# Kernel tuning notes

Hardware: AMD Instinct MI355X
Metric: run time of the kernel (lower is better)

## Reference

```python
import jax, jax.numpy as jnp
import numpy as np

EMBED_DIM = 1024
NUM_HEADS = 16
HEAD_DIM = EMBED_DIM // NUM_HEADS


def setup_inputs() -> dict:
    key = jax.random.key(0)
    ks = jax.random.split(key, 11)
    B, T, D = 4, 2048, EMBED_DIM
    s = 1.0 / np.sqrt(D)
    inp = {
        "x": jax.random.normal(ks[0], (B, T, D), dtype=jnp.float32),
        "wq": jax.random.normal(ks[1], (D, D), dtype=jnp.float32) * s,
        "bq": jnp.zeros((D,), dtype=jnp.float32),
        "wk": jax.random.normal(ks[2], (D, D), dtype=jnp.float32) * s,
        "bk": jnp.zeros((D,), dtype=jnp.float32),
        "wv": jax.random.normal(ks[3], (D, D), dtype=jnp.float32) * s,
        "bv": jnp.zeros((D,), dtype=jnp.float32),
        "wo": jax.random.normal(ks[4], (D, D), dtype=jnp.float32) * s,
        "bo": jnp.zeros((D,), dtype=jnp.float32),
        "ln_gamma": jnp.ones((D,), dtype=jnp.float32),
        "ln_beta": jnp.zeros((D,), dtype=jnp.float32),
    }
    return inp


def _attention(x, wq, bq, wk, bk, wv, bv, wo, bo, ln_gamma, ln_beta):
    B, T, D = x.shape
    H, Hd = NUM_HEADS, HEAD_DIM
    # projections -> (B, H, T, Hd)
    q = (x @ wq + bq).reshape(B, T, H, Hd).transpose(0, 2, 1, 3)
    k = (x @ wk + bk).reshape(B, T, H, Hd).transpose(0, 2, 1, 3)
    v = (x @ wv + bv).reshape(B, T, H, Hd).transpose(0, 2, 1, 3)
    scores = jnp.einsum("bhqd,bhkd->bhqk", q, k) / jnp.sqrt(jnp.asarray(Hd, x.dtype))
    attn = jax.nn.softmax(scores, axis=-1)  # dropout p=0 -> identity
    out = jnp.einsum("bhqk,bhkd->bhqd", attn, v)
    out = out.transpose(0, 2, 1, 3).reshape(B, T, D)
    out = out @ wo + bo
    # LayerNorm (no residual in the original forward)
    mu = jnp.mean(out, axis=-1, keepdims=True)
    var = jnp.var(out, axis=-1, keepdims=True)
    out = (out - mu) / jnp.sqrt(var + 1e-5) * ln_gamma + ln_beta
    return out


def reference(x, wq, bq, wk, bk, wv, bv, wo, bo, ln_gamma, ln_beta):
    return _attention(x, wq, bq, wk, bk, wv, bv, wo, bo, ln_gamma, ln_beta)
```

## Files before the change

kernel.cpp:

```cpp
#include <hip/hip_runtime.h>
#include <hip/hip_bf16.h>

typedef __bf16 bf16_t;
typedef __bf16 bf16x4v __attribute__((ext_vector_type(4)));
typedef __bf16 bf16x8 __attribute__((ext_vector_type(8)));
typedef float  f32x4  __attribute__((ext_vector_type(4)));

typedef __attribute__((address_space(1))) void* gptr_t;
typedef __attribute__((address_space(3))) void* lptr_t;

#define B_BATCH  4
#define T_SEQ    2048
#define D_MODEL  1024
#define N_HEADS  16
#define HEAD_DIM 64
#define M_ROWS   (B_BATCH * T_SEQ)

#define PROW 40

#define EXP2_SCALE 0.1803368801111204f

__global__ __launch_bounds__(256) void cvt_x(
    const float* __restrict__ in, bf16_t* __restrict__ out)
{
    const size_t tid = (size_t)blockIdx.x * 256 + threadIdx.x;
    for (int rep = 0; rep < 4; rep++) {
        const size_t i = (tid + (size_t)rep * 524288) * 4;
        const f32x4 v = *(const f32x4*)&in[i];
        bf16x4v o;
        for (int e = 0; e < 4; e++) o[e] = (bf16_t)v[e];
        *(bf16x4v*)&out[i] = o;
    }
}

__global__ __launch_bounds__(256) void transpose_w(
    const float* __restrict__ w0, const float* __restrict__ w1,
    const float* __restrict__ w2, const float* __restrict__ w3,
    bf16_t* __restrict__ out)
{
    __shared__ bf16_t tile[32][33];
    const int z = blockIdx.z;
    const float* w = (z == 0) ? w0 : (z == 1) ? w1 : (z == 2) ? w2 : w3;
    bf16_t* o = out + (size_t)z * D_MODEL * D_MODEL;
    const int tx = threadIdx.x & 31, ty = threadIdx.x >> 5;
    const int k0 = blockIdx.y * 32, n0 = blockIdx.x * 32;
    for (int i = 0; i < 4; i++)
        tile[ty + i * 8][tx] = (bf16_t)w[(size_t)(k0 + ty + i * 8) * D_MODEL + n0 + tx];
    __syncthreads();
    for (int i = 0; i < 4; i++)
        o[(size_t)(n0 + ty + i * 8) * D_MODEL + k0 + tx] = tile[tx][ty + i * 8];
}

__global__ __launch_bounds__(512, 2) void qkv_k(
    const bf16_t* __restrict__ A, const bf16_t* __restrict__ BT,
    const float* __restrict__ bq, const float* __restrict__ bk,
    const float* __restrict__ bv,
    bf16_t* __restrict__ qk_out, bf16_t* __restrict__ vt_out)
{
    __shared__ __attribute__((aligned(16))) bf16_t smem[49152];

    const int tid = threadIdx.x;
    const int f0 = blockIdx.y * 24 + blockIdx.x;
    const int f  = (f0 & 7) * 96 + (f0 >> 3);
    const int n_t = f % 24, m_t = f / 24;
    const int m0 = m_t * 256, n0 = n_t * 128;
    const int z  = n0 >> 10;
    const int w = tid >> 6, lane = tid & 63, quad = lane >> 4, l16 = lane & 15;
    const int wm = w >> 1, wn = w & 1;
    const int srow = lane >> 3;
    const int scol = ((lane & 7) ^ srow) * 8;
    const int rx = l16 & 7;

    f32x4 acc[4][4] = {};

    for (int it = 0; it < 4; it++) {
        const int R = w * 32 + it * 8;
        __builtin_amdgcn_global_load_lds(
            (gptr_t)&A[(size_t)(m0 + R + srow) * D_MODEL + scol],
            (lptr_t)&smem[R * 64], 16, 0, 0);
    }
    for (int it = 0; it < 2; it++) {
        const int R = w * 16 + it * 8;
        __builtin_amdgcn_global_load_lds(
            (gptr_t)&BT[(size_t)(n0 + R + srow) * D_MODEL + scol],
            (lptr_t)&smem[32768 + R * 64], 16, 0, 0);
    }

    for (int t = 0; t < 16; t++) {
        __syncthreads();
        const bf16_t* Ac = &smem[(t & 1) * 16384];
        const bf16_t* Bc = &smem[32768 + (t & 1) * 8192];
        bf16_t* An = &smem[((t + 1) & 1) * 16384];
        bf16_t* Bn = &smem[32768 + ((t + 1) & 1) * 8192];
        const int kb = (t + 1) * 64;
        const bool pf = (t + 1 < 16);

        #pragma unroll
        for (int s = 0; s < 2; s++) {
            const int rc = ((quad + s * 4) ^ rx) * 8;
            bf16x8 bfr[4];
            #pragma unroll
            for (int j = 0; j < 4; j++)
                bfr[j] = *(const bf16x8*)&Bc[(wn * 64 + j * 16 + l16) * 64 + rc];
            if (pf) {
                const int RA0 = w * 32 + (s * 2) * 8;
                __builtin_amdgcn_global_load_lds(
                    (gptr_t)&A[(size_t)(m0 + RA0 + srow) * D_MODEL + kb + scol],
                    (lptr_t)&An[RA0 * 64], 16, 0, 0);
                const int RA1 = w * 32 + (s * 2 + 1) * 8;
                __builtin_amdgcn_global_load_lds(
                    (gptr_t)&A[(size_t)(m0 + RA1 + srow) * D_MODEL + kb + scol],
                    (lptr_t)&An[RA1 * 64], 16, 0, 0);
                const int RB = w * 16 + s * 8;
                __builtin_amdgcn_global_load_lds(
                    (gptr_t)&BT[(size_t)(n0 + RB + srow) * D_MODEL + kb + scol],
                    (lptr_t)&Bn[RB * 64], 16, 0, 0);
            }
            bf16x8 af[4];
            #pragma unroll
            for (int i = 0; i < 4; i++)
                af[i] = *(const bf16x8*)&Ac[(wm * 64 + i * 16 + l16) * 64 + rc];
            __builtin_amdgcn_s_setprio(1);
            #pragma unroll
            for (int i = 0; i < 4; i++)
                #pragma unroll
                for (int j = 0; j < 4; j++)
                    acc[i][j] = __builtin_amdgcn_mfma_f32_16x16x32_bf16(
                        af[i], bfr[j], acc[i][j], 0, 0, 0);
            __builtin_amdgcn_s_setprio(0);
        }
    }

    __syncthreads();

    const float* bias = (z == 0) ? bq : (z == 1) ? bk : bv;
    const float qscale = (z == 0) ? EXP2_SCALE : 1.0f;
    const int ncol0 = n0 & 1023;
    float bj[4];
    for (int j = 0; j < 4; j++)
        bj[j] = bias[ncol0 + wn * 64 + j * 16 + l16];

    const int bidx = m0 >> 11, t0 = m0 & 2047, hbase = ncol0 >> 6;
    if (z < 2) {
        bf16_t (*Cs)[136] = reinterpret_cast<bf16_t(*)[136]>(smem);
        for (int ai = 0; ai < 4; ai++)
            for (int r = 0; r < 4; r++) {
                const int row = wm * 64 + ai * 16 + quad * 4 + r;
                for (int j = 0; j < 4; j++)
                    Cs[row][wn * 64 + j * 16 + l16] =
                        (bf16_t)((acc[ai][j][r] + bj[j]) * qscale);
            }
        __syncthreads();
        bf16_t* outp = qk_out + (size_t)z * ((size_t)M_ROWS * D_MODEL);
        for (int p = 0; p < 8; p++) {
            const int chunk = p * 512 + tid;
            const int sub = chunk & 15, tt = chunk >> 4;
            const int hl = sub >> 3, sub8 = sub & 7;
            const bf16x8 val = *(const bf16x8*)&Cs[tt][hl * 64 + sub8 * 8];
            *(bf16x8*)&outp[(((size_t)(bidx * N_HEADS + hbase + hl)) * T_SEQ + t0 + tt)
                            * HEAD_DIM + sub8 * 8] = val;
        }
    } else {
        bf16_t (*CsV)[264] = reinterpret_cast<bf16_t(*)[264]>(smem);
        for (int ai = 0; ai < 4; ai++)
            for (int r = 0; r < 4; r++) {
                const int row = wm * 64 + ai * 16 + quad * 4 + r;
                for (int j = 0; j < 4; j++)
                    CsV[wn * 64 + j * 16 + l16][row] = (bf16_t)(acc[ai][j][r] + bj[j]);
            }
        __syncthreads();
        for (int p = 0; p < 8; p++) {
            const int chunk = p * 512 + tid;
            const int sub = chunk & 31, r = chunk >> 5;
            const int h = hbase + (r >> 6), hd = r & 63;
            const bf16x8 val = *(const bf16x8*)&CsV[r][sub * 8];
            *(bf16x8*)&vt_out[(((size_t)(bidx * N_HEADS + h)) * HEAD_DIM + hd) * T_SEQ
                              + t0 + sub * 8] = val;
        }
    }
}

__global__ __launch_bounds__(512, 2) void proj_k(
    const bf16_t* __restrict__ A, const bf16_t* __restrict__ BT,
    const float* __restrict__ bias, float* __restrict__ out)
{
    __shared__ __attribute__((aligned(16))) bf16_t smem[49152];

    const int tid = threadIdx.x;
    const int f0 = blockIdx.y * 8 + blockIdx.x;
    const int f  = (f0 & 7) * 32 + (f0 >> 3);
    const int n_t = f & 7, m_t = f >> 3;
    const int m0 = m_t * 256, n0 = n_t * 128;
    const int w = tid >> 6, lane = tid & 63, quad = lane >> 4, l16 = lane & 15;
    const int wm = w >> 1, wn = w & 1;
    const int srow = lane >> 3;
    const int scol = ((lane & 7) ^ srow) * 8;
    const int rx = l16 & 7;

    f32x4 acc[4][4] = {};

    for (int it = 0; it < 4; it++) {
        const int R = w * 32 + it * 8;
        __builtin_amdgcn_global_load_lds(
            (gptr_t)&A[(size_t)(m0 + R + srow) * D_MODEL + scol],
            (lptr_t)&smem[R * 64], 16, 0, 0);
    }
    for (int it = 0; it < 2; it++) {
        const int R = w * 16 + it * 8;
        __builtin_amdgcn_global_load_lds(
            (gptr_t)&BT[(size_t)(n0 + R + srow) * D_MODEL + scol],
            (lptr_t)&smem[32768 + R * 64], 16, 0, 0);
    }

    for (int t = 0; t < 16; t++) {
        __syncthreads();
        const bf16_t* Ac = &smem[(t & 1) * 16384];
        const bf16_t* Bc = &smem[32768 + (t & 1) * 8192];
        bf16_t* An = &smem[((t + 1) & 1) * 16384];
        bf16_t* Bn = &smem[32768 + ((t + 1) & 1) * 8192];
        const int kb = (t + 1) * 64;
        const bool pf = (t + 1 < 16);

        #pragma unroll
        for (int s = 0; s < 2; s++) {
            const int rc = ((quad + s * 4) ^ rx) * 8;
            bf16x8 bfr[4];
            #pragma unroll
            for (int j = 0; j < 4; j++)
                bfr[j] = *(const bf16x8*)&Bc[(wn * 64 + j * 16 + l16) * 64 + rc];
            if (pf) {
                const int RA0 = w * 32 + (s * 2) * 8;
                __builtin_amdgcn_global_load_lds(
                    (gptr_t)&A[(size_t)(m0 + RA0 + srow) * D_MODEL + kb + scol],
                    (lptr_t)&An[RA0 * 64], 16, 0, 0);
                const int RA1 = w * 32 + (s * 2 + 1) * 8;
                __builtin_amdgcn_global_load_lds(
                    (gptr_t)&A[(size_t)(m0 + RA1 + srow) * D_MODEL + kb + scol],
                    (lptr_t)&An[RA1 * 64], 16, 0, 0);
                const int RB = w * 16 + s * 8;
                __builtin_amdgcn_global_load_lds(
                    (gptr_t)&BT[(size_t)(n0 + RB + srow) * D_MODEL + kb + scol],
                    (lptr_t)&Bn[RB * 64], 16, 0, 0);
            }
            bf16x8 af[4];
            #pragma unroll
            for (int i = 0; i < 4; i++)
                af[i] = *(const bf16x8*)&Ac[(wm * 64 + i * 16 + l16) * 64 + rc];
            __builtin_amdgcn_s_setprio(1);
            #pragma unroll
            for (int i = 0; i < 4; i++)
                #pragma unroll
                for (int j = 0; j < 4; j++)
                    acc[i][j] = __builtin_amdgcn_mfma_f32_16x16x32_bf16(
                        af[i], bfr[j], acc[i][j], 0, 0, 0);
            __builtin_amdgcn_s_setprio(0);
        }
    }

    float bj[4];
    for (int j = 0; j < 4; j++)
        bj[j] = bias[n0 + wn * 64 + j * 16 + l16];

    for (int i = 0; i < 4; i++)
        for (int r = 0; r < 4; r++) {
            const int rg = m0 + wm * 64 + i * 16 + quad * 4 + r;
            for (int j = 0; j < 4; j++) {
                const int cg = n0 + wn * 64 + j * 16 + l16;
                out[(size_t)rg * D_MODEL + cg] = acc[i][j][r] + bj[j];
            }
        }
}

__global__ __launch_bounds__(256, 4) void attn_k(
    const bf16_t* __restrict__ Q, const bf16_t* __restrict__ K,
    const bf16_t* __restrict__ VT, bf16_t* __restrict__ O)
{
    __shared__ __attribute__((aligned(16))) bf16_t Ks[2][64 * 64];
    __shared__ __attribute__((aligned(16))) bf16_t Vs[64 * 64];
    __shared__ __attribute__((aligned(16))) bf16_t Ps[4][32][PROW];

    const int tid = threadIdx.x;
    const int f = blockIdx.y * 16 + blockIdx.x;
    const int xcd = f & 7, j = f >> 3;
    const int bh = xcd * 8 + (j & 7);
    const int qbase = (j >> 3) * 128;
    const int b = bh >> 4, h = bh & 15;
    const int w = tid >> 6, lane = tid & 63, quad = lane >> 4, l16 = lane & 15;
    const size_t head_off = (size_t)bh * T_SEQ * HEAD_DIM;
    const bf16_t* Qh  = Q  + head_off;
    const bf16_t* Kh  = K  + head_off;
    const bf16_t* VTh = VT + head_off;

    const int srow = lane >> 3;
    const int scol = ((lane & 7) ^ srow) * 8;

    const int rxor = l16 & 7;
    const int rc0 = ((0 + quad) ^ rxor) * 8;
    const int rc1 = ((4 + quad) ^ rxor) * 8;

    bf16x8 bq[2][2];
    for (int iq = 0; iq < 2; iq++)
        for (int s = 0; s < 2; s++)
            bq[iq][s] = *(const bf16x8*)
                &Qh[(size_t)(qbase + w * 32 + iq * 16 + l16) * HEAD_DIM + s * 32 + quad * 8];

    bf16x8 vone;
    for (int e = 0; e < 8; e++) vone[e] = (bf16_t)1.0f;

    for (int it = 0; it < 2; it++) {
        const int R = w * 16 + it * 8;
        __builtin_amdgcn_global_load_lds(
            (gptr_t)&Kh[(size_t)(R + srow) * HEAD_DIM + scol],
            (lptr_t)&Ks[0][R * 64], 16, 0, 0);
    }

    f32x4 Oacc[2][4] = {};
    f32x4 lacc[2] = {};

    for (int kt = 0; kt < T_SEQ / 64; kt++) {
        const int kbase = kt * 64;
        __syncthreads();
        const bf16_t* Kc = Ks[kt & 1];

        for (int it = 0; it < 2; it++) {
            const int R = w * 16 + it * 8;
            __builtin_amdgcn_global_load_lds(
                (gptr_t)&VTh[(size_t)(R + srow) * T_SEQ + kbase + scol],
                (lptr_t)&Vs[R * 64], 16, 0, 0);
        }
        if (kt + 1 < T_SEQ / 64) {
            bf16_t* Kn = Ks[(kt + 1) & 1];
            for (int it = 0; it < 2; it++) {
                const int R = w * 16 + it * 8;
                __builtin_amdgcn_global_load_lds(
                    (gptr_t)&Kh[(size_t)(kbase + 64 + R + srow) * HEAD_DIM + scol],
                    (lptr_t)&Kn[R * 64], 16, 0, 0);
            }
        }

        f32x4 St[4][2] = {};
        for (int s = 0; s < 2; s++) {
            const int rc = s ? rc1 : rc0;
            bf16x8 ak[4];
            for (int jk = 0; jk < 4; jk++)
                ak[jk] = *(const bf16x8*)&Kc[(jk * 16 + l16) * 64 + rc];
            __builtin_amdgcn_s_setprio(1);
            for (int jk = 0; jk < 4; jk++)
                for (int iq = 0; iq < 2; iq++)
                    St[jk][iq] = __builtin_amdgcn_mfma_f32_16x16x32_bf16(
                        ak[jk], bq[iq][s], St[jk][iq], 0, 0, 0);
            __builtin_amdgcn_s_setprio(0);
        }

        for (int kk = 0; kk < 2; kk++)
            for (int iq = 0; iq < 2; iq++) {
                bf16x4v pv;
                for (int r = 0; r < 4; r++)
                    pv[r] = (bf16_t)__builtin_amdgcn_exp2f(St[kk][iq][r]);
                *(bf16x4v*)&Ps[w][iq * 16 + l16][kk * 16 + quad * 4] = pv;
            }
        asm volatile("" ::: "memory");

        __syncthreads();

        {
            bf16x8 ap[2], bv4[4];
            for (int iq = 0; iq < 2; iq++)
                ap[iq] = *(const bf16x8*)&Ps[w][iq * 16 + l16][quad * 8];
            for (int jn = 0; jn < 4; jn++)
                bv4[jn] = *(const bf16x8*)&Vs[(jn * 16 + l16) * 64 + rc0];
            __builtin_amdgcn_s_setprio(1);
            for (int iq = 0; iq < 2; iq++) {
                for (int jn = 0; jn < 4; jn++)
                    Oacc[iq][jn] = __builtin_amdgcn_mfma_f32_16x16x32_bf16(
                        ap[iq], bv4[jn], Oacc[iq][jn], 0, 0, 0);
                lacc[iq] = __builtin_amdgcn_mfma_f32_16x16x32_bf16(
                    ap[iq], vone, lacc[iq], 0, 0, 0);
            }
            __builtin_amdgcn_s_setprio(0);
        }

        for (int kk = 0; kk < 2; kk++)
            for (int iq = 0; iq < 2; iq++) {
                bf16x4v pv;
                for (int r = 0; r < 4; r++)
                    pv[r] = (bf16_t)__builtin_amdgcn_exp2f(St[2 + kk][iq][r]);
                *(bf16x4v*)&Ps[w][iq * 16 + l16][kk * 16 + quad * 4] = pv;
            }
        asm volatile("" ::: "memory");

        {
            bf16x8 ap[2], bv4[4];
            for (int iq = 0; iq < 2; iq++)
                ap[iq] = *(const bf16x8*)&Ps[w][iq * 16 + l16][quad * 8];
            for (int jn = 0; jn < 4; jn++)
                bv4[jn] = *(const bf16x8*)&Vs[(jn * 16 + l16) * 64 + rc1];
            __builtin_amdgcn_s_setprio(1);
            for (int iq = 0; iq < 2; iq++) {
                for (int jn = 0; jn < 4; jn++)
                    Oacc[iq][jn] = __builtin_amdgcn_mfma_f32_16x16x32_bf16(
                        ap[iq], bv4[jn], Oacc[iq][jn], 0, 0, 0);
                lacc[iq] = __builtin_amdgcn_mfma_f32_16x16x32_bf16(
                    ap[iq], vone, lacc[iq], 0, 0, 0);
            }
            __builtin_amdgcn_s_setprio(0);
        }
    }

    for (int iq = 0; iq < 2; iq++) {
        for (int r = 0; r < 4; r++) {
            const float inv = 1.f / lacc[iq][r];
            const int t = qbase + w * 32 + iq * 16 + quad * 4 + r;
            for (int jn = 0; jn < 4; jn++) {
                const int hd = jn * 16 + l16;
                O[(((size_t)(b * T_SEQ + t)) * N_HEADS + h) * HEAD_DIM + hd] =
                    (bf16_t)(Oacc[iq][jn][r] * inv);
            }
        }
    }
}

__global__ __launch_bounds__(256) void ln_k(
    const float* __restrict__ proj, const float* __restrict__ gamma,
    const float* __restrict__ beta, float* __restrict__ out)
{
    const int tid = threadIdx.x;
    const int w = tid >> 6, lane = tid & 63;
    const int row = blockIdx.x * 4 + w;
    const float* p = proj + (size_t)row * D_MODEL;
    f32x4 v[4];
    float s1 = 0.f, s2 = 0.f;
    for (int e = 0; e < 4; e++) {
        v[e] = *(const f32x4*)&p[e * 256 + lane * 4];
        for (int k = 0; k < 4; k++) { s1 += v[e][k]; s2 += v[e][k] * v[e][k]; }
    }
    for (int off = 32; off >= 1; off >>= 1) {
        s1 += __shfl_xor(s1, off, 64);
        s2 += __shfl_xor(s2, off, 64);
    }
    const float mu  = s1 * (1.f / D_MODEL);
    const float var = s2 * (1.f / D_MODEL) - mu * mu;
    const float rstd = rsqrtf(var + 1e-5f);
    float* o = out + (size_t)row * D_MODEL;
    for (int e = 0; e < 4; e++) {
        const int c = e * 256 + lane * 4;
        const f32x4 g4 = *(const f32x4*)&gamma[c];
        const f32x4 b4 = *(const f32x4*)&beta[c];
        f32x4 ov;
        for (int k = 0; k < 4; k++) ov[k] = (v[e][k] - mu) * rstd * g4[k] + b4[k];
        *(f32x4*)&o[c] = ov;
    }
}

extern "C" void kernel_launch(void* const* d_in, const int* in_sizes, int n_in,
                              void* d_out, int out_size, void* d_ws, size_t ws_size,
                              hipStream_t stream)
{
    const float* x  = (const float*)d_in[0];
    const float* wq = (const float*)d_in[1];
    const float* bq = (const float*)d_in[2];
    const float* wk = (const float*)d_in[3];
    const float* bk = (const float*)d_in[4];
    const float* wv = (const float*)d_in[5];
    const float* bv = (const float*)d_in[6];
    const float* wo = (const float*)d_in[7];
    const float* bo = (const float*)d_in[8];
    const float* g  = (const float*)d_in[9];
    const float* be = (const float*)d_in[10];

    char* ws = (char*)d_ws;
    bf16_t* xb   = (bf16_t*)(ws);
    bf16_t* wT   = (bf16_t*)(ws + ((size_t)16 << 20));
    bf16_t* qkv  = (bf16_t*)(ws + ((size_t)24 << 20));
    bf16_t* attn = (bf16_t*)(ws + ((size_t)72 << 20));
    float*  proj = (float*) (ws + ((size_t)88 << 20));
    bf16_t* vt   = (bf16_t*)proj;

    cvt_x<<<dim3(2048), 256, 0, stream>>>(x, xb);
    transpose_w<<<dim3(32, 32, 4), 256, 0, stream>>>(wq, wk, wv, wo, wT);

    qkv_k<<<dim3(24, 32), 512, 0, stream>>>(xb, wT, bq, bk, bv, qkv, vt);

    bf16_t* Qm = qkv;
    bf16_t* Km = qkv + (size_t)M_ROWS * D_MODEL;

    attn_k<<<dim3(16, 64), 256, 0, stream>>>(Qm, Km, vt, attn);

    proj_k<<<dim3(8, 32), 512, 0, stream>>>(
        attn, wT + (size_t)3 * D_MODEL * D_MODEL, bo, (float*)proj);

    ln_k<<<dim3(M_ROWS / 4), 256, 0, stream>>>(proj, g, be, (float*)d_out);
}
```

Baseline: 274.6 us.

## Fuse prep kernels, hoist GEMM prefetch, and fuse projection with LayerNorm via grid sync

Merges the x conversion and weight transposes into one launch. In the QKV and output-projection GEMMs, all next-tile prefetches are issued once at the top of each k-step instead of interleaved between MFMA sub-steps. It also fuses the output projection and LayerNorm into a single cooperative kernel that syncs the whole grid before normalising rows. This removes two launches and their tail gaps, but the cooperative launch requires all 256 blocks to be resident, and launch bounds drop to one block per CU.

```diff
diff --git a/kernel.cpp b/kernel.cpp
--- a/kernel.cpp
+++ b/kernel.cpp
@@ -1,5 +1,8 @@
 #include <hip/hip_runtime.h>
 #include <hip/hip_bf16.h>
+#include <hip/hip_cooperative_groups.h>
+
+namespace cg = cooperative_groups;
 
 typedef __bf16 bf16_t;
 typedef __bf16 bf16x4v __attribute__((ext_vector_type(4)));
@@ -20,35 +23,36 @@
 
 #define EXP2_SCALE 0.1803368801111204f
 
-__global__ __launch_bounds__(256) void cvt_x(
-    const float* __restrict__ in, bf16_t* __restrict__ out)
-{
-    const size_t tid = (size_t)blockIdx.x * 256 + threadIdx.x;
-    for (int rep = 0; rep < 4; rep++) {
-        const size_t i = (tid + (size_t)rep * 524288) * 4;
-        const f32x4 v = *(const f32x4*)&in[i];
-        bf16x4v o;
-        for (int e = 0; e < 4; e++) o[e] = (bf16_t)v[e];
-        *(bf16x4v*)&out[i] = o;
-    }
-}
-
-__global__ __launch_bounds__(256) void transpose_w(
-    const float* __restrict__ w0, const float* __restrict__ w1,
-    const float* __restrict__ w2, const float* __restrict__ w3,
-    bf16_t* __restrict__ out)
+__global__ __launch_bounds__(256) void prep_k(
+    const float* __restrict__ x, const float* __restrict__ w0,
+    const float* __restrict__ w1, const float* __restrict__ w2,
+    const float* __restrict__ w3,
+    bf16_t* __restrict__ xb, bf16_t* __restrict__ wT)
 {
     __shared__ bf16_t tile[32][33];
-    const int z = blockIdx.z;
-    const float* w = (z == 0) ? w0 : (z == 1) ? w1 : (z == 2) ? w2 : w3;
-    bf16_t* o = out + (size_t)z * D_MODEL * D_MODEL;
-    const int tx = threadIdx.x & 31, ty = threadIdx.x >> 5;
-    const int k0 = blockIdx.y * 32, n0 = blockIdx.x * 32;
-    for (int i = 0; i < 4; i++)
-        tile[ty + i * 8][tx] = (bf16_t)w[(size_t)(k0 + ty + i * 8) * D_MODEL + n0 + tx];
-    __syncthreads();
-    for (int i = 0; i < 4; i++)
-        o[(size_t)(n0 + ty + i * 8) * D_MODEL + k0 + tx] = tile[tx][ty + i * 8];
+    const int bid = blockIdx.x;
+    if (bid < 4096) {
+        const int z = bid >> 10, rem = bid & 1023;
+        const int n0 = (rem & 31) * 32, k0 = (rem >> 5) * 32;
+        const float* w = (z == 0) ? w0 : (z == 1) ? w1 : (z == 2) ? w2 : w3;
+        bf16_t* o = wT + (size_t)z * D_MODEL * D_MODEL;
+        const int tx = threadIdx.x & 31, ty = threadIdx.x >> 5;
+        for (int i = 0; i < 4; i++)
+            tile[ty + i * 8][tx] =
+                (bf16_t)w[(size_t)(k0 + ty + i * 8) * D_MODEL + n0 + tx];
+        __syncthreads();
+        for (int i = 0; i < 4; i++)
+            o[(size_t)(n0 + ty + i * 8) * D_MODEL + k0 + tx] = tile[tx][ty + i * 8];
+    } else {
+        const size_t tid = (size_t)(bid - 4096) * 256 + threadIdx.x;
+        for (int rep = 0; rep < 4; rep++) {
+            const size_t i = (tid + (size_t)rep * 524288) * 4;
+            const f32x4 v = *(const f32x4*)&x[i];
+            bf16x4v o;
+            for (int e = 0; e < 4; e++) o[e] = (bf16_t)v[e];
+            *(bf16x4v*)&xb[i] = o;
+        }
+    }
 }
 
 __global__ __launch_bounds__(512, 2) void qkv_k(
@@ -93,7 +97,23 @@
         bf16_t* An = &smem[((t + 1) & 1) * 16384];
         bf16_t* Bn = &smem[32768 + ((t + 1) & 1) * 8192];
         const int kb = (t + 1) * 64;
-        const bool pf = (t + 1 < 16);
+
+        if (t + 1 < 16) {
+            #pragma unroll
+            for (int it = 0; it < 4; it++) {
+                const int R = w * 32 + it * 8;
+                __builtin_amdgcn_global_load_lds(
+                    (gptr_t)&A[(size_t)(m0 + R + srow) * D_MODEL + kb + scol],
+                    (lptr_t)&An[R * 64], 16, 0, 0);
+            }
+            #pragma unroll
+            for (int it = 0; it < 2; it++) {
+                const int R = w * 16 + it * 8;
+                __builtin_amdgcn_global_load_lds(
+                    (gptr_t)&BT[(size_t)(n0 + R + srow) * D_MODEL + kb + scol],
+                    (lptr_t)&Bn[R * 64], 16, 0, 0);
+            }
+        }
 
         #pragma unroll
         for (int s = 0; s < 2; s++) {
@@ -102,20 +122,6 @@
             #pragma unroll
             for (int j = 0; j < 4; j++)
                 bfr[j] = *(const bf16x8*)&Bc[(wn * 64 + j * 16 + l16) * 64 + rc];
-            if (pf) {
-                const int RA0 = w * 32 + (s * 2) * 8;
-                __builtin_amdgcn_global_load_lds(
-                    (gptr_t)&A[(size_t)(m0 + RA0 + srow) * D_MODEL + kb + scol],
-                    (lptr_t)&An[RA0 * 64], 16, 0, 0);
-                const int RA1 = w * 32 + (s * 2 + 1) * 8;
-                __builtin_amdgcn_global_load_lds(
-                    (gptr_t)&A[(size_t)(m0 + RA1 + srow) * D_MODEL + kb + scol],
-                    (lptr_t)&An[RA1 * 64], 16, 0, 0);
-                const int RB = w * 16 + s * 8;
-                __builtin_amdgcn_global_load_lds(
-                    (gptr_t)&BT[(size_t)(n0 + RB + srow) * D_MODEL + kb + scol],
-                    (lptr_t)&Bn[RB * 64], 16, 0, 0);
-            }
             bf16x8 af[4];
             #pragma unroll
             for (int i = 0; i < 4; i++)
@@ -180,14 +186,16 @@
     }
 }
 
-__global__ __launch_bounds__(512, 2) void proj_k(
+__global__ __launch_bounds__(512, 1) void projln_k(
     const bf16_t* __restrict__ A, const bf16_t* __restrict__ BT,
-    const float* __restrict__ bias, float* __restrict__ out)
+    const float* __restrict__ bias, float* __restrict__ proj,
+    const float* __restrict__ gamma, const float* __restrict__ beta,
+    float* __restrict__ out)
 {
     __shared__ __attribute__((aligned(16))) bf16_t smem[49152];
 
     const int tid = threadIdx.x;
-    const int f0 = blockIdx.y * 8 + blockIdx.x;
+    const int f0 = blockIdx.x;
     const int f  = (f0 & 7) * 32 + (f0 >> 3);
     const int n_t = f & 7, m_t = f >> 3;
     const int m0 = m_t * 256, n0 = n_t * 128;
@@ -219,7 +227,23 @@
         bf16_t* An = &smem[((t + 1) & 1) * 16384];
         bf16_t* Bn = &smem[32768 + ((t + 1) & 1) * 8192];
         const int kb = (t + 1) * 64;
-        const bool pf = (t + 1 < 16);
+
+        if (t + 1 < 16) {
+            #pragma unroll
+            for (int it = 0; it < 4; it++) {
+                const int R = w * 32 + it * 8;
+                __builtin_amdgcn_global_load_lds(
+                    (gptr_t)&A[(size_t)(m0 + R + srow) * D_MODEL + kb + scol],
+                    (lptr_t)&An[R * 64], 16, 0, 0);
+            }
+            #pragma unroll
+            for (int it = 0; it < 2; it++) {
+                const int R = w * 16 + it * 8;
+                __builtin_amdgcn_global_load_lds(
+                    (gptr_t)&BT[(size_t)(n0 + R + srow) * D_MODEL + kb + scol],
+                    (lptr_t)&Bn[R * 64], 16, 0, 0);
+            }
+        }
 
         #pragma unroll
         for (int s = 0; s < 2; s++) {
@@ -228,20 +252,6 @@
             #pragma unroll
             for (int j = 0; j < 4; j++)
                 bfr[j] = *(const bf16x8*)&Bc[(wn * 64 + j * 16 + l16) * 64 + rc];
-            if (pf) {
-                const int RA0 = w * 32 + (s * 2) * 8;
-                __builtin_amdgcn_global_load_lds(
-                    (gptr_t)&A[(size_t)(m0 + RA0 + srow) * D_MODEL + kb + scol],
-                    (lptr_t)&An[RA0 * 64], 16, 0, 0);
-                const int RA1 = w * 32 + (s * 2 + 1) * 8;
-                __builtin_amdgcn_global_load_lds(
-                    (gptr_t)&A[(size_t)(m0 + RA1 + srow) * D_MODEL + kb + scol],
-                    (lptr_t)&An[RA1 * 64], 16, 0, 0);
-                const int RB = w * 16 + s * 8;
-                __builtin_amdgcn_global_load_lds(
-                    (gptr_t)&BT[(size_t)(n0 + RB + srow) * D_MODEL + kb + scol],
-                    (lptr_t)&Bn[RB * 64], 16, 0, 0);
-            }
             bf16x8 af[4];
             #pragma unroll
             for (int i = 0; i < 4; i++)
@@ -266,9 +276,40 @@
             const int rg = m0 + wm * 64 + i * 16 + quad * 4 + r;
             for (int j = 0; j < 4; j++) {
                 const int cg = n0 + wn * 64 + j * 16 + l16;
-                out[(size_t)rg * D_MODEL + cg] = acc[i][j][r] + bj[j];
-            }
-        }
+                proj[(size_t)rg * D_MODEL + cg] = acc[i][j][r] + bj[j];
+            }
+        }
+
+    __threadfence();
+    cg::this_grid().sync();
+
+    const int row0 = f0 * 32 + w * 4;
+    for (int rr = 0; rr < 4; rr++) {
+        const int row = row0 + rr;
+        const float* p = proj + (size_t)row * D_MODEL;
+        f32x4 v[4];
+        float s1 = 0.f, s2 = 0.f;
+        for (int e = 0; e < 4; e++) {
+            v[e] = *(const f32x4*)&p[e * 256 + lane * 4];
+            for (int k = 0; k < 4; k++) { s1 += v[e][k]; s2 += v[e][k] * v[e][k]; }
+        }
+        for (int off = 32; off >= 1; off >>= 1) {
+            s1 += __shfl_xor(s1, off, 64);
+            s2 += __shfl_xor(s2, off, 64);
+        }
+        const float mu  = s1 * (1.f / D_MODEL);
+        const float var = s2 * (1.f / D_MODEL) - mu * mu;
+        const float rstd = rsqrtf(var + 1e-5f);
+        float* o = out + (size_t)row * D_MODEL;
+        for (int e = 0; e < 4; e++) {
+            const int c = e * 256 + lane * 4;
+            const f32x4 g4 = *(const f32x4*)&gamma[c];
+            const f32x4 b4 = *(const f32x4*)&beta[c];
+            f32x4 ov;
+            for (int k = 0; k < 4; k++) ov[k] = (v[e][k] - mu) * rstd * g4[k] + b4[k];
+            *(f32x4*)&o[c] = ov;
+        }
+    }
 }
 
 __global__ __launch_bounds__(256, 4) void attn_k(
@@ -417,38 +458,6 @@
                     (bf16_t)(Oacc[iq][jn][r] * inv);
             }
         }
-    }
-}
-
-__global__ __launch_bounds__(256) void ln_k(
-    const float* __restrict__ proj, const float* __restrict__ gamma,
-    const float* __restrict__ beta, float* __restrict__ out)
-{
-    const int tid = threadIdx.x;
-    const int w = tid >> 6, lane = tid & 63;
-    const int row = blockIdx.x * 4 + w;
-    const float* p = proj + (size_t)row * D_MODEL;
-    f32x4 v[4];
-    float s1 = 0.f, s2 = 0.f;
-    for (int e = 0; e < 4; e++) {
-        v[e] = *(const f32x4*)&p[e * 256 + lane * 4];
-        for (int k = 0; k < 4; k++) { s1 += v[e][k]; s2 += v[e][k] * v[e][k]; }
-    }
-    for (int off = 32; off >= 1; off >>= 1) {
-        s1 += __shfl_xor(s1, off, 64);
-        s2 += __shfl_xor(s2, off, 64);
-    }
-    const float mu  = s1 * (1.f / D_MODEL);
-    const float var = s2 * (1.f / D_MODEL) - mu * mu;
-    const float rstd = rsqrtf(var + 1e-5f);
-    float* o = out + (size_t)row * D_MODEL;
-    for (int e = 0; e < 4; e++) {
-        const int c = e * 256 + lane * 4;
-        const f32x4 g4 = *(const f32x4*)&gamma[c];
-        const f32x4 b4 = *(const f32x4*)&beta[c];
-        f32x4 ov;
-        for (int k = 0; k < 4; k++) ov[k] = (v[e][k] - mu) * rstd * g4[k] + b4[k];
-        *(f32x4*)&o[c] = ov;
     }
 }
 
@@ -476,8 +485,7 @@
     float*  proj = (float*) (ws + ((size_t)88 << 20));
     bf16_t* vt   = (bf16_t*)proj;
 
-    cvt_x<<<dim3(2048), 256, 0, stream>>>(x, xb);
-    transpose_w<<<dim3(32, 32, 4), 256, 0, stream>>>(wq, wk, wv, wo, wT);
+    prep_k<<<dim3(6144), 256, 0, stream>>>(x, wq, wk, wv, wo, xb, wT);
 
     qkv_k<<<dim3(24, 32), 512, 0, stream>>>(xb, wT, bq, bk, bv, qkv, vt);
 
@@ -486,8 +494,17 @@
 
     attn_k<<<dim3(16, 64), 256, 0, stream>>>(Qm, Km, vt, attn);
 
-    proj_k<<<dim3(8, 32), 512, 0, stream>>>(
-        attn, wT + (size_t)3 * D_MODEL * D_MODEL, bo, (float*)proj);
-
-    ln_k<<<dim3(M_ROWS / 4), 256, 0, stream>>>(proj, g, be, (float*)d_out);
+    {
+        const bf16_t* pa = attn;
+        const bf16_t* pb = wT + (size_t)3 * D_MODEL * D_MODEL;
+        const float*  pbias = bo;
+        float* pproj = proj;
+        const float* pg = g;
+        const float* pbe = be;
+        float* pout = (float*)d_out;
+        void* args[] = {(void*)&pa, (void*)&pb, (void*)&pbias, (void*)&pproj,
+                        (void*)&pg, (void*)&pbe, (void*)&pout};
+        hipLaunchCooperativeKernel((void*)projln_k, dim3(256), dim3(512),
+                                   args, 0, stream);
+    }
 }
```

After: 396.3 us. +44.3%, slower.
